# Performance work log

Measured on AMD Instinct MI355X. Metric: run time of the kernel, lower is better.

Reference implementation:

```python
import jax, jax.numpy as jnp
import numpy as np

N = 50000        # nodes
E = 400000       # edges
CHUNK = 100      # per-modality input dim
NCH = 2          # number of chunks (modalities)
OUT = 96         # out_chunks
HID = NCH * OUT  # m_hidden = 192
NCLS = 2         # edge classes
EPS = 1e-5


def layer_norm(x, g, b):
    m = jnp.mean(x, axis=-1, keepdims=True)
    v = jnp.var(x, axis=-1, keepdims=True)
    return (x - m) * jax.lax.rsqrt(v + EPS) * g + b


def setup_inputs() -> dict:
    key = jax.random.key(0)
    ks = jax.random.split(key, 20)
    inp = {}
    inp["h"] = jax.random.normal(ks[0], (N, NCH * CHUNK), dtype=jnp.float32)
    inp["dist"] = jax.random.uniform(ks[1], (E,), dtype=jnp.float32)
    inp["src"] = jax.random.randint(ks[2], (E,), 0, N)
    inp["dst"] = jax.random.randint(ks[3], (E,), 0, N)
    # projector params (equal chunk sizes -> stacked): Linear(100,96)+LayerNorm(96)
    s = 1.0 / np.sqrt(CHUNK)
    inp["proj_W"] = jax.random.uniform(ks[4], (NCH, CHUNK, OUT), minval=-s, maxval=s, dtype=jnp.float32)
    inp["proj_b"] = jax.random.uniform(ks[5], (NCH, OUT), minval=-s, maxval=s, dtype=jnp.float32)
    inp["proj_g"] = jnp.ones((NCH, OUT), jnp.float32)
    inp["proj_beta"] = jnp.zeros((NCH, OUT), jnp.float32)
    # 2 GcnSAGE layers actually run (m_layers-1): Linear(2*192, 192) + LayerNorm(192)
    sg = 1.0 / np.sqrt(2 * HID)
    inp["gcn_W"] = jax.random.uniform(ks[6], (2, 2 * HID, HID), minval=-sg, maxval=sg, dtype=jnp.float32)
    inp["gcn_b"] = jax.random.uniform(ks[7], (2, HID), minval=-sg, maxval=sg, dtype=jnp.float32)
    inp["gcn_g"] = jnp.ones((2, HID), jnp.float32)
    inp["gcn_beta"] = jnp.zeros((2, HID), jnp.float32)
    # edge MLP predictor: 192 -> 96 -> 2
    s1 = 1.0 / np.sqrt(HID)
    s2 = 1.0 / np.sqrt(HID // 2)
    inp["ep_W1"] = jax.random.uniform(ks[8], (HID, HID // 2), minval=-s1, maxval=s1, dtype=jnp.float32)
    inp["ep_b1"] = jax.random.uniform(ks[9], (HID // 2,), minval=-s1, maxval=s1, dtype=jnp.float32)
    inp["ep_W2"] = jax.random.uniform(ks[10], (HID // 2, NCLS), minval=-s2, maxval=s2, dtype=jnp.float32)
    inp["ep_b2"] = jax.random.uniform(ks[11], (NCLS,), minval=-s2, maxval=s2, dtype=jnp.float32)
    return inp


def reference(h, dist, proj_W, proj_b, proj_g, proj_beta,
              gcn_W, gcn_b, gcn_g, gcn_beta,
              ep_W1, ep_b1, ep_W2, ep_b2, src, dst):
    # InputProjector: per-chunk Linear + LayerNorm + LeakyReLU, concat
    x = h.reshape(N, NCH, CHUNK)
    y = jnp.einsum('ncd,cde->nce', x, proj_W) + proj_b
    y = jax.nn.leaky_relu(layer_norm(y, proj_g, proj_beta), negative_slope=0.01)
    hh = y.reshape(N, HID)

    # 1/in_degree norm (inf -> 0)
    deg = jax.ops.segment_sum(jnp.ones((E,), hh.dtype), dst, num_segments=N)
    norm = jnp.where(deg > 0, 1.0 / deg, 0.0)[:, None]

    # m_layers - 1 = 2 GcnSAGE layers: ah = sum_{u->v} h_u * dist_e
    for l in range(2):
        msg = hh[src] * dist[:, None]                       # [E, HID]
        ah = jax.ops.segment_sum(msg, dst, num_segments=N)  # [N, HID]
        hc = jnp.concatenate([hh, ah * norm], axis=1)       # [N, 2*HID]
        hh = hc @ gcn_W[l] + gcn_b[l]
        hh = jax.nn.relu(layer_norm(hh, gcn_g[l], gcn_beta[l]))

    # edge scoring: W2(relu(W1(h_src * h_dst)))
    he = hh[src] * hh[dst]                                   # [E, HID]
    score = jax.nn.relu(he @ ep_W1 + ep_b1) @ ep_W2 + ep_b2  # [E, 2]
    return score
```

## Files before the change

kernel.cpp:

```cpp
#include <hip/hip_runtime.h>
#include <math.h>

#define N_NODES 50000
#define N_EDGES 400000
#define CHUNK   100
#define NCH     2
#define OUTC    96
#define HID     192
#define HID2    384
#define EPS     1e-5f

typedef __bf16 bf16x8 __attribute__((ext_vector_type(8)));
typedef float  f32x4  __attribute__((ext_vector_type(4)));

__device__ inline unsigned short f2bf(float f) {
    unsigned int u = __float_as_uint(f);
    unsigned int r = (u + 0x7FFFu + ((u >> 16) & 1u)) >> 16;
    return (unsigned short)r;
}

#define W1T_SZ (96 * 192)
__global__ void prep_w1t(const float* __restrict__ W1, unsigned short* __restrict__ w1t)
{
    int i = blockIdx.x * 256 + threadIdx.x;
    if (i < W1T_SZ) {
        int j = i / HID, k = i % HID;
        w1t[i] = f2bf(W1[k * OUTC + j]);
    }
}

__global__ __launch_bounds__(192) void proj_kernel(
    const float* __restrict__ h, const float* __restrict__ W,
    const float* __restrict__ b, const float* __restrict__ g,
    const float* __restrict__ beta, float* __restrict__ hh)
{
    __shared__ float xs[16][NCH * CHUNK];
    __shared__ float red[2][16][2][6];
    __shared__ float mv[2][16][2];
    const int tid = threadIdx.x;
    const int nbase = blockIdx.x * 16;

    for (int i = tid; i < 16 * 50; i += 192) {
        int row = i / 50, seg = i % 50;
        int n = nbase + row;
        float4 v = make_float4(0.f, 0.f, 0.f, 0.f);
        if (n < N_NODES) v = *(const float4*)&h[(size_t)n * (NCH * CHUNK) + seg * 4];
        *(float4*)&xs[row][seg * 4] = v;
    }
    __syncthreads();

    const int c = tid / OUTC, j = tid % OUTC;
    const float* wc = &W[c * CHUNK * OUTC];

    float acc[16];
    float bb = b[c * OUTC + j];
    #pragma unroll
    for (int i = 0; i < 16; ++i) acc[i] = bb;

    for (int d = 0; d < CHUNK; d += 4) {
        float w0 = wc[(d + 0) * OUTC + j];
        float w1 = wc[(d + 1) * OUTC + j];
        float w2 = wc[(d + 2) * OUTC + j];
        float w3 = wc[(d + 3) * OUTC + j];
        #pragma unroll
        for (int i = 0; i < 16; ++i) {
            float4 hv = *(const float4*)&xs[i][c * CHUNK + d];
            acc[i] += hv.x * w0 + hv.y * w1 + hv.z * w2 + hv.w * w3;
        }
    }
    __syncthreads();
    float* ys = &xs[0][0];
    #pragma unroll
    for (int i = 0; i < 16; ++i) ys[i * HID + c * OUTC + j] = acc[i];
    __syncthreads();
    {
        int grp = tid / 6, q = tid % 6;
        int gi = grp >> 1, gc = grp & 1;
        float s = 0.f, s2 = 0.f;
        #pragma unroll
        for (int t = 0; t < 16; ++t) {
            float v = ys[gi * HID + gc * OUTC + q + 6 * t];
            s += v; s2 += v * v;
        }
        red[0][gi][gc][q] = s; red[1][gi][gc][q] = s2;
    }
    __syncthreads();
    if (tid < 32) {
        int gi = tid >> 1, gc = tid & 1;
        float s = 0.f, s2 = 0.f;
        #pragma unroll
        for (int q = 0; q < 6; ++q) { s += red[0][gi][gc][q]; s2 += red[1][gi][gc][q]; }
        float mean = s * (1.f / 96.f);
        float var  = s2 * (1.f / 96.f) - mean * mean;
        mv[0][gi][gc] = mean;
        mv[1][gi][gc] = rsqrtf(var + EPS);
    }
    __syncthreads();
    float gg = g[c * OUTC + j], be = beta[c * OUTC + j];
    #pragma unroll
    for (int i = 0; i < 16; ++i) {
        int n = nbase + i;
        if (n < N_NODES) {
            float y = (acc[i] - mv[0][i][c]) * mv[1][i][c] * gg + be;
            y = (y < 0.f) ? 0.01f * y : y;
            hh[(size_t)n * HID + c * OUTC + j] = y;
        }
    }
}

__global__ void zero_deg_kernel(int* __restrict__ deg)
{
    int i = blockIdx.x * blockDim.x + threadIdx.x;
    if (i < N_NODES) deg[i] = 0;
}

__global__ void count_kernel(const int* __restrict__ dst, int* __restrict__ deg)
{
    int e = blockIdx.x * blockDim.x + threadIdx.x;
    if (e < N_EDGES) atomicAdd(&deg[dst[e]], 1);
}

__global__ __launch_bounds__(1024) void scan_kernel(
    const int* __restrict__ deg, int* __restrict__ rowstart,
    int* __restrict__ cursor, float* __restrict__ norm)
{
    __shared__ int sums[1024];
    const int t = threadIdx.x;
    const int L = (N_NODES + 1023) / 1024;
    int lo = t * L, hi = min(lo + L, N_NODES);
    int s = 0;
    for (int i = lo; i < hi; ++i) s += deg[i];
    sums[t] = s;
    __syncthreads();
    if (t == 0) {
        int run = 0;
        for (int i = 0; i < 1024; ++i) { int v = sums[i]; sums[i] = run; run += v; }
        rowstart[N_NODES] = run;
    }
    __syncthreads();
    int off = sums[t];
    for (int i = lo; i < hi; ++i) {
        int d = deg[i];
        rowstart[i] = off;
        cursor[i]   = off;
        norm[i]     = (d > 0) ? 1.f / (float)d : 0.f;
        off += d;
    }
}

__global__ void fill_kernel(const int* __restrict__ src, const int* __restrict__ dst,
                            const float* __restrict__ dist, int* __restrict__ cursor,
                            int* __restrict__ eidx, int* __restrict__ csr_src,
                            float* __restrict__ csr_dist)
{
    int e = blockIdx.x * blockDim.x + threadIdx.x;
    if (e < N_EDGES) {
        int pos = atomicAdd(&cursor[dst[e]], 1);
        eidx[pos]     = e;
        csr_src[pos]  = src[e];
        csr_dist[pos] = dist[e];
    }
}

__global__ __launch_bounds__(256) void aggregate_kernel(
    const float* __restrict__ hh, const int* __restrict__ csr_src,
    const float* __restrict__ csr_dist, const int* __restrict__ rowstart,
    const float* __restrict__ norm, float* __restrict__ ahn)
{
    const int wave = threadIdx.x >> 6;
    const int lane = threadIdx.x & 63;
    const int v = blockIdx.x * 4 + wave;
    if (v >= N_NODES) return;
    const int r0 = rowstart[v], r1 = rowstart[v + 1];
    float a0 = 0.f, a1 = 0.f, a2 = 0.f;
    int k = r0;
    for (; k + 1 < r1; k += 2) {
        int   s0 = csr_src[k],      s1 = csr_src[k + 1];
        float d0 = csr_dist[k],     d1 = csr_dist[k + 1];
        const float* h0 = &hh[(size_t)s0 * HID];
        const float* h1 = &hh[(size_t)s1 * HID];
        a0 += h0[lane]       * d0 + h1[lane]       * d1;
        a1 += h0[lane + 64]  * d0 + h1[lane + 64]  * d1;
        a2 += h0[lane + 128] * d0 + h1[lane + 128] * d1;
    }
    if (k < r1) {
        int s0 = csr_src[k];
        float d0 = csr_dist[k];
        const float* h0 = &hh[(size_t)s0 * HID];
        a0 += h0[lane] * d0; a1 += h0[lane + 64] * d0; a2 += h0[lane + 128] * d0;
    }
    float nm = norm[v];
    ahn[(size_t)v * HID + lane]       = a0 * nm;
    ahn[(size_t)v * HID + lane + 64]  = a1 * nm;
    ahn[(size_t)v * HID + lane + 128] = a2 * nm;
}

__global__ __launch_bounds__(192) void update_kernel(
    float* __restrict__ hh, const float* __restrict__ ahn,
    const float* __restrict__ W, const float* __restrict__ b,
    const float* __restrict__ g, const float* __restrict__ beta)
{
    __shared__ float hcs[16][HID2];
    __shared__ float red[2][16][12];
    __shared__ float mv[2][16];
    const int tid = threadIdx.x;
    const int nbase = blockIdx.x * 16;

    for (int i = 0; i < 16; ++i) {
        int n = nbase + i;
        hcs[i][tid]       = hh[(size_t)n * HID + tid];
        hcs[i][HID + tid] = ahn[(size_t)n * HID + tid];
    }
    __syncthreads();

    float acc[16];
    float bb0 = b[tid];
    #pragma unroll
    for (int i = 0; i < 16; ++i) acc[i] = bb0;

    for (int d = 0; d < HID2; d += 4) {
        float w0 = W[(d + 0) * HID + tid];
        float w1 = W[(d + 1) * HID + tid];
        float w2 = W[(d + 2) * HID + tid];
        float w3 = W[(d + 3) * HID + tid];
        #pragma unroll
        for (int i = 0; i < 16; ++i) {
            float4 hv = *(const float4*)&hcs[i][d];
            acc[i] += hv.x * w0 + hv.y * w1 + hv.z * w2 + hv.w * w3;
        }
    }
    __syncthreads();
    float* ys = &hcs[0][0];
    #pragma unroll
    for (int i = 0; i < 16; ++i) ys[i * HID + tid] = acc[i];
    __syncthreads();
    {
        int i = tid / 12, j = tid % 12;
        float s = 0.f, s2 = 0.f;
        for (int k = j; k < HID; k += 12) { float v = ys[i * HID + k]; s += v; s2 += v * v; }
        red[0][i][j] = s; red[1][i][j] = s2;
    }
    __syncthreads();
    if (tid < 16) {
        float s = 0.f, s2 = 0.f;
        for (int j = 0; j < 12; ++j) { s += red[0][tid][j]; s2 += red[1][tid][j]; }
        float mean = s * (1.f / HID);
        float var  = s2 * (1.f / HID) - mean * mean;
        mv[0][tid] = mean;
        mv[1][tid] = rsqrtf(var + EPS);
    }
    __syncthreads();
    float gg = g[tid], be = beta[tid];
    #pragma unroll
    for (int i = 0; i < 16; ++i) {
        float y = (acc[i] - mv[0][i]) * mv[1][i] * gg + be;
        hh[(size_t)(nbase + i) * HID + tid] = (y > 0.f) ? y : 0.f;
    }
}

__global__ __launch_bounds__(256) void edge_mfma_kernel(
    const float* __restrict__ hh, const int* __restrict__ src, const int* __restrict__ dst,
    const int* __restrict__ eidx,
    const unsigned short* __restrict__ w1t, const float* __restrict__ b1,
    const float* __restrict__ W2, const float* __restrict__ b2,
    float* __restrict__ out)
{
    __shared__ unsigned short he[64][200];
    __shared__ int sidx[64], didx[64], eor[64];
    const int tid = threadIdx.x;
    const int ebase = blockIdx.x * 64;

    if (tid < 64) {
        int e = eidx[ebase + tid];
        eor[tid] = e;
        sidx[tid] = src[e];
        didx[tid] = dst[e];
    }
    __syncthreads();

    const int w    = tid >> 6;
    const int lane = tid & 63;
    const int lo   = lane & 15;
    const int hi   = lane >> 4;

    for (int i = 0; i < 16; ++i) {
        int slot = w * 16 + i;
        const float* hs = &hh[(size_t)sidx[slot] * HID];
        const float* hd = &hh[(size_t)didx[slot] * HID];
        float p0 = hs[lane]       * hd[lane];
        float p1 = hs[lane + 64]  * hd[lane + 64];
        float p2 = hs[lane + 128] * hd[lane + 128];
        he[slot][lane]       = f2bf(p0);
        he[slot][lane + 64]  = f2bf(p1);
        he[slot][lane + 128] = f2bf(p2);
    }

    f32x4 acc[6];
    #pragma unroll
    for (int nt = 0; nt < 6; ++nt) acc[nt] = (f32x4){0.f, 0.f, 0.f, 0.f};

    #pragma unroll
    for (int kt = 0; kt < 6; ++kt) {
        const int k0 = kt * 32 + hi * 8;
        bf16x8 af = *(const bf16x8*)&he[w * 16 + lo][k0];
        #pragma unroll
        for (int nt = 0; nt < 6; ++nt) {
            bf16x8 bfr = *(const bf16x8*)&w1t[(size_t)(nt * 16 + lo) * HID + k0];
            acc[nt] = __builtin_amdgcn_mfma_f32_16x16x32_bf16(af, bfr, acc[nt], 0, 0, 0);
        }
    }

    float b1c[6], w20[6], w21[6];
    #pragma unroll
    for (int nt = 0; nt < 6; ++nt) {
        int col = nt * 16 + lo;
        b1c[nt] = b1[col];
        w20[nt] = W2[col * 2 + 0];
        w21[nt] = W2[col * 2 + 1];
    }
    float bb0 = b2[0], bb1 = b2[1];
    #pragma unroll
    for (int reg = 0; reg < 4; ++reg) {
        float p0 = 0.f, p1 = 0.f;
        #pragma unroll
        for (int nt = 0; nt < 6; ++nt) {
            float hv = fmaxf(acc[nt][reg] + b1c[nt], 0.f);
            p0 += hv * w20[nt];
            p1 += hv * w21[nt];
        }
        #pragma unroll
        for (int off = 1; off < 16; off <<= 1) {
            p0 += __shfl_xor(p0, off, 64);
            p1 += __shfl_xor(p1, off, 64);
        }
        if (lo == 0) {
            int row = hi * 4 + reg;
            int e = eor[w * 16 + row];
            out[(size_t)e * 2 + 0] = p0 + bb0;
            out[(size_t)e * 2 + 1] = p1 + bb1;
        }
    }
}

extern "C" void kernel_launch(void* const* d_in, const int* in_sizes, int n_in,
                              void* d_out, int out_size, void* d_ws, size_t ws_size,
                              hipStream_t stream)
{
    const float* h         = (const float*)d_in[0];
    const float* dist      = (const float*)d_in[1];
    const int*   src       = (const int*)  d_in[2];
    const int*   dst       = (const int*)  d_in[3];
    const float* proj_W    = (const float*)d_in[4];
    const float* proj_b    = (const float*)d_in[5];
    const float* proj_g    = (const float*)d_in[6];
    const float* proj_beta = (const float*)d_in[7];
    const float* gcn_W     = (const float*)d_in[8];
    const float* gcn_b     = (const float*)d_in[9];
    const float* gcn_g     = (const float*)d_in[10];
    const float* gcn_beta  = (const float*)d_in[11];
    const float* ep_W1     = (const float*)d_in[12];
    const float* ep_b1     = (const float*)d_in[13];
    const float* ep_W2     = (const float*)d_in[14];
    const float* ep_b2     = (const float*)d_in[15];
    float* out = (float*)d_out;

    char* p = (char*)d_ws;
    float* hh  = (float*)p;  p += (size_t)N_NODES * HID * sizeof(float);
    float* ahn = (float*)p;  p += (size_t)N_NODES * HID * sizeof(float);
    float* nrm = (float*)p;  p += (size_t)N_NODES * sizeof(float);
    int* deg      = (int*)p; p += (size_t)N_NODES * sizeof(int);
    int* rowstart = (int*)p; p += (size_t)(N_NODES + 1) * sizeof(int);
    int* cursor   = (int*)p; p += (size_t)N_NODES * sizeof(int);
    int* eidx     = (int*)p; p += (size_t)N_EDGES * sizeof(int);
    int* csr_src  = (int*)p; p += (size_t)N_EDGES * sizeof(int);
    float* csr_dist = (float*)p; p += (size_t)N_EDGES * sizeof(float);
    p = (char*)(((uintptr_t)p + 255) & ~(uintptr_t)255);
    unsigned short* w1t = (unsigned short*)p; p += (size_t)W1T_SZ * sizeof(unsigned short);

    prep_w1t<<<(W1T_SZ + 255) / 256, 256, 0, stream>>>(ep_W1, w1t);
    proj_kernel<<<(N_NODES + 15) / 16, 192, 0, stream>>>(
        h, proj_W, proj_b, proj_g, proj_beta, hh);
    zero_deg_kernel<<<(N_NODES + 255) / 256, 256, 0, stream>>>(deg);
    count_kernel<<<(N_EDGES + 255) / 256, 256, 0, stream>>>(dst, deg);
    scan_kernel<<<1, 1024, 0, stream>>>(deg, rowstart, cursor, nrm);
    fill_kernel<<<(N_EDGES + 255) / 256, 256, 0, stream>>>(
        src, dst, dist, cursor, eidx, csr_src, csr_dist);
    for (int l = 0; l < 2; ++l) {
        aggregate_kernel<<<(N_NODES + 3) / 4, 256, 0, stream>>>(
            hh, csr_src, csr_dist, rowstart, nrm, ahn);
        update_kernel<<<N_NODES / 16, 192, 0, stream>>>(
            hh, ahn, gcn_W + (size_t)l * HID2 * HID, gcn_b + l * HID,
            gcn_g + l * HID, gcn_beta + l * HID);
    }
    edge_mfma_kernel<<<N_EDGES / 64, 256, 0, stream>>>(
        hh, src, dst, eidx, w1t, ep_b1, ep_W2, ep_b2, out);
}
```

Measured before the change: 831.1 us.

## Use single-wavefront update kernel with 3 outputs per thread and shuffle LayerNorm

The GCN update kernel now runs with one 64-thread wavefront per block, and each thread computes three output columns for 16 nodes, so each shared-memory row load is reused three times. The LayerNorm reduction now uses wave-level xor shuffles instead of shared-memory partial sums with several barriers, and the node tile is loaded with float4 accesses. In exchange, each thread holds 48 accumulators, which raises register pressure, and each block has only one wave, which may leave latency poorly hidden.

```diff
diff --git a/kernel.cpp b/kernel.cpp
--- a/kernel.cpp
+++ b/kernel.cpp
@@ -195,66 +195,70 @@
     ahn[(size_t)v * HID + lane + 128] = a2 * nm;
 }
 
-__global__ __launch_bounds__(192) void update_kernel(
+__global__ __launch_bounds__(64) void update_kernel(
     float* __restrict__ hh, const float* __restrict__ ahn,
     const float* __restrict__ W, const float* __restrict__ b,
     const float* __restrict__ g, const float* __restrict__ beta)
 {
-    __shared__ float hcs[16][HID2];
-    __shared__ float red[2][16][12];
-    __shared__ float mv[2][16];
+    __shared__ float xs[16][HID2];
     const int tid = threadIdx.x;
     const int nbase = blockIdx.x * 16;
 
+    for (int i = tid; i < 16 * 96; i += 64) {
+        int row = i / 96, seg = i % 96;
+        int n = nbase + row;
+        float4 v = (seg < 48) ? *(const float4*)&hh[(size_t)n * HID + seg * 4]
+                              : *(const float4*)&ahn[(size_t)n * HID + (seg - 48) * 4];
+        *(float4*)&xs[row][seg * 4] = v;
+    }
+    __syncthreads();
+
+    float acc[16][3];
+    {
+        float bb0 = b[tid], bb1 = b[tid + 64], bb2 = b[tid + 128];
+        #pragma unroll
+        for (int i = 0; i < 16; ++i) { acc[i][0] = bb0; acc[i][1] = bb1; acc[i][2] = bb2; }
+    }
+
+    #pragma unroll 2
+    for (int d = 0; d < HID2; d += 4) {
+        float wv[4][3];
+        #pragma unroll
+        for (int q = 0; q < 4; ++q) {
+            const float* wr = &W[(size_t)(d + q) * HID + tid];
+            wv[q][0] = wr[0]; wv[q][1] = wr[64]; wv[q][2] = wr[128];
+        }
+        #pragma unroll
+        for (int i = 0; i < 16; ++i) {
+            float4 hv = *(const float4*)&xs[i][d];
+            #pragma unroll
+            for (int c = 0; c < 3; ++c)
+                acc[i][c] += hv.x * wv[0][c] + hv.y * wv[1][c] + hv.z * wv[2][c] + hv.w * wv[3][c];
+        }
+    }
+
+    float gg0 = g[tid], gg1 = g[tid + 64], gg2 = g[tid + 128];
+    float be0 = beta[tid], be1 = beta[tid + 64], be2 = beta[tid + 128];
+
+    #pragma unroll
     for (int i = 0; i < 16; ++i) {
-        int n = nbase + i;
-        hcs[i][tid]       = hh[(size_t)n * HID + tid];
-        hcs[i][HID + tid] = ahn[(size_t)n * HID + tid];
-    }
-    __syncthreads();
-
-    float acc[16];
-    float bb0 = b[tid];
-    #pragma unroll
-    for (int i = 0; i < 16; ++i) acc[i] = bb0;
-
-    for (int d = 0; d < HID2; d += 4) {
-        float w0 = W[(d + 0) * HID + tid];
-        float w1 = W[(d + 1) * HID + tid];
-        float w2 = W[(d + 2) * HID + tid];
-        float w3 = W[(d + 3) * HID + tid];
-        #pragma unroll
-        for (int i = 0; i < 16; ++i) {
-            float4 hv = *(const float4*)&hcs[i][d];
-            acc[i] += hv.x * w0 + hv.y * w1 + hv.z * w2 + hv.w * w3;
-        }
-    }
-    __syncthreads();
-    float* ys = &hcs[0][0];
-    #pragma unroll
-    for (int i = 0; i < 16; ++i) ys[i * HID + tid] = acc[i];
-    __syncthreads();
-    {
-        int i = tid / 12, j = tid % 12;
-        float s = 0.f, s2 = 0.f;
-        for (int k = j; k < HID; k += 12) { float v = ys[i * HID + k]; s += v; s2 += v * v; }
-        red[0][i][j] = s; red[1][i][j] = s2;
-    }
-    __syncthreads();
-    if (tid < 16) {
-        float s = 0.f, s2 = 0.f;
-        for (int j = 0; j < 12; ++j) { s += red[0][tid][j]; s2 += red[1][tid][j]; }
+        float s  = acc[i][0] + acc[i][1] + acc[i][2];
+        float s2 = acc[i][0] * acc[i][0] + acc[i][1] * acc[i][1] + acc[i][2] * acc[i][2];
+        #pragma unroll
+        for (int off = 1; off < 64; off <<= 1) {
+            s  += __shfl_xor(s,  off, 64);
+            s2 += __shfl_xor(s2, off, 64);
+        }
         float mean = s * (1.f / HID);
         float var  = s2 * (1.f / HID) - mean * mean;
-        mv[0][tid] = mean;
-        mv[1][tid] = rsqrtf(var + EPS);
-    }
-    __syncthreads();
-    float gg = g[tid], be = beta[tid];
-    #pragma unroll
-    for (int i = 0; i < 16; ++i) {
-        float y = (acc[i] - mv[0][i]) * mv[1][i] * gg + be;
-        hh[(size_t)(nbase + i) * HID + tid] = (y > 0.f) ? y : 0.f;
+        float rstd = rsqrtf(var + EPS);
+        float* hn = &hh[(size_t)(nbase + i) * HID + tid];
+        float y0 = (acc[i][0] - mean) * rstd * gg0 + be0;
+        float y1 = (acc[i][1] - mean) * rstd * gg1 + be1;
+        float y2 = (acc[i][2] - mean) * rstd * gg2 + be2;
+        hn[0]   = (y0 > 0.f) ? y0 : 0.f;
+        hn[64]  = (y1 > 0.f) ? y1 : 0.f;
+        hn[128] = (y2 > 0.f) ? y2 : 0.f;
     }
 }
 
@@ -388,7 +392,7 @@
     for (int l = 0; l < 2; ++l) {
         aggregate_kernel<<<(N_NODES + 3) / 4, 256, 0, stream>>>(
             hh, csr_src, csr_dist, rowstart, nrm, ahn);
-        update_kernel<<<N_NODES / 16, 192, 0, stream>>>(
+        update_kernel<<<N_NODES / 16, 64, 0, stream>>>(
             hh, ahn, gcn_W + (size_t)l * HID2 * HID, gcn_b + l * HID,
             gcn_g + l * HID, gcn_beta + l * HID);
     }
```

Measured after the change: 1.180 ms. +42.0%, slower.
